# Kernel optimization log

Measured on AMD Instinct MI355X. Metric: run time of the kernel, lower is better.

## Reference

```python
import jax, jax.numpy as jnp
import numpy as np

B, S, D = 4, 1024, 2048
H, KVH = 32, 8
HD = D // H            # 64
KVD = HD * KVH         # 512
RANK, ALPHA = 16, 32
LORA_SCALE = ALPHA / RANK


def setup_inputs() -> dict:
    key = jax.random.key(0)
    ks = jax.random.split(key, 14)
    x = jax.random.normal(ks[0], (B, S, D), dtype=jnp.float32)
    # RoPE tables (llama-style complex freqs as cos/sin)
    inv = 1.0 / (10000.0 ** (np.arange(0, HD, 2, dtype=np.float32) / HD))
    t = np.arange(S, dtype=np.float32)
    ang = np.outer(t, inv)  # [S, HD//2]
    freqs_cos = jnp.asarray(np.cos(ang))
    freqs_sin = jnp.asarray(np.sin(ang))
    s = 0.02
    Wq = jax.random.normal(ks[1], (D, D), dtype=jnp.float32) * s
    Wk = jax.random.normal(ks[2], (D, KVD), dtype=jnp.float32) * s
    Wv = jax.random.normal(ks[3], (D, KVD), dtype=jnp.float32) * s
    Wo = jax.random.normal(ks[4], (D, D), dtype=jnp.float32) * s
    qA = jax.random.normal(ks[5], (D, RANK), dtype=jnp.float32) * s
    qB = jax.random.normal(ks[6], (RANK, D), dtype=jnp.float32) * s
    kA = jax.random.normal(ks[7], (D, RANK), dtype=jnp.float32) * s
    kB = jax.random.normal(ks[8], (RANK, KVD), dtype=jnp.float32) * s
    vA = jax.random.normal(ks[9], (D, RANK), dtype=jnp.float32) * s
    vB = jax.random.normal(ks[10], (RANK, KVD), dtype=jnp.float32) * s
    return {"x": x, "freqs_cos": freqs_cos, "freqs_sin": freqs_sin,
            "Wq": Wq, "Wk": Wk, "Wv": Wv, "Wo": Wo,
            "qA": qA, "qB": qB, "kA": kA, "kB": kB, "vA": vA, "vB": vB}


def _rope(t, cos, sin):
    # t: [b, s, h, hd]; cos/sin: [s, hd//2]
    b, s, h, hd = t.shape
    t2 = t.reshape(b, s, h, hd // 2, 2)
    x0, x1 = t2[..., 0], t2[..., 1]
    c = cos[None, :, None, :]
    sn = sin[None, :, None, :]
    r0 = x0 * c - x1 * sn
    r1 = x0 * sn + x1 * c
    return jnp.stack([r0, r1], axis=-1).reshape(b, s, h, hd)


def reference(x, freqs_cos, freqs_sin, Wq, Wk, Wv, Wo, qA, qB, kA, kB, vA, vB):
    b, s, _ = x.shape
    # QKV projections + LoRA deltas
    q = x @ Wq + (x @ qA) @ qB * LORA_SCALE   # [b,s,D]
    k = x @ Wk + (x @ kA) @ kB * LORA_SCALE   # [b,s,KVD]
    v = x @ Wv + (x @ vA) @ vB * LORA_SCALE   # [b,s,KVD]
    q = q.reshape(b, s, H, HD)
    k = k.reshape(b, s, KVH, HD)
    v = v.reshape(b, s, KVH, HD)
    q = _rope(q, freqs_cos, freqs_sin)
    k = _rope(k, freqs_cos, freqs_sin)
    # GQA attention without materializing repeated K/V:
    rep = H // KVH
    qg = q.reshape(b, s, KVH, rep, HD)
    scale = 1.0 / jnp.sqrt(jnp.asarray(HD, dtype=x.dtype))
    scores = jnp.einsum('bsgrd,btgd->bgrst', qg, k) * scale  # [b,kvh,rep,s,s]
    causal = jnp.tril(jnp.ones((s, s), dtype=bool))
    scores = jnp.where(causal[None, None, None], scores, jnp.finfo(scores.dtype).min)
    attn = jax.nn.softmax(scores, axis=-1)
    ctx = jnp.einsum('bgrst,btgd->bsgrd', attn, v).reshape(b, s, D)
    return ctx @ Wo
```

## Files before the change

### kernel.cpp

```cpp
#include <hip/hip_runtime.h>

typedef unsigned short u16;
typedef unsigned int u32;
typedef __attribute__((ext_vector_type(8))) short short8;
typedef __attribute__((ext_vector_type(4))) float f32x4;
typedef __attribute__((ext_vector_type(4))) u16 u16x4;

#define LOG2E 1.4426950408889634f
#define SCL2 (0.125f * LOG2E)

static __device__ __forceinline__ float bf2f(u16 u) {
    return __uint_as_float(((unsigned)u) << 16);
}
static __device__ __forceinline__ u16 f2bf(float f) {
    unsigned u = __float_as_uint(f);
    unsigned r = (u + 0x7FFF + ((u >> 16) & 1)) >> 16;
    return (u16)r;
}
static __device__ __forceinline__ u32 cvtpk(float lo, float hi) {
    u32 r;
    asm("v_cvt_pk_bf16_f32 %0, %1, %2" : "=v"(r) : "v"(lo), "v"(hi));
    return r;
}
static __device__ __forceinline__ f32x4 mfma16(short8 a, short8 b, f32x4 c) {
    return __builtin_amdgcn_mfma_f32_16x16x32_bf16(a, b, c, 0, 0, 0);
}
static __device__ __forceinline__ void gload_lds16(const void* g, void* l) {
    __builtin_amdgcn_global_load_lds(
        (const __attribute__((address_space(1))) void*)g,
        (__attribute__((address_space(3))) void*)l, 16, 0, 0);
}

#define GBAR() do { asm volatile("" ::: "memory"); __builtin_amdgcn_s_barrier(); asm volatile("" ::: "memory"); } while (0)
#define LGW()  do { asm volatile("s_waitcnt lgkmcnt(0)" ::: "memory"); __builtin_amdgcn_sched_barrier(0); } while (0)

__global__ void cast_pack_kernel(const float* __restrict__ x, u16* __restrict__ xb,
                                 const float* __restrict__ cosb, const float* __restrict__ sinb,
                                 u32* __restrict__ tbl) {
    if (blockIdx.x >= 2048) {
        const int i = (blockIdx.x - 2048) * 1024 + threadIdx.x * 4;
#pragma unroll
        for (int j = 0; j < 4; ++j)
            tbl[i + j] = (u32)f2bf(cosb[i + j]) | ((u32)f2bf(sinb[i + j]) << 16);
        return;
    }
    constexpr int n = 4096 * 2048;
    constexpr int stride = 2048 * 256 * 4;
    int i = (blockIdx.x * 256 + threadIdx.x) * 4;
#pragma unroll
    for (; i < n; i += stride) {
        f32x4 v = *(const f32x4*)&x[i];
        u16x4 o;
        o.x = f2bf(v.x); o.y = f2bf(v.y); o.z = f2bf(v.z); o.w = f2bf(v.w);
        *(u16x4*)&xb[i] = o;
    }
}

__global__ void prep_weights_kernel(
    const float* __restrict__ Wq, const float* __restrict__ Wk,
    const float* __restrict__ Wv, const float* __restrict__ Wo,
    const float* __restrict__ qA, const float* __restrict__ qB,
    const float* __restrict__ kA, const float* __restrict__ kB,
    const float* __restrict__ vA, const float* __restrict__ vB,
    u16* __restrict__ WqkvT, u16* __restrict__ WoT) {
    __shared__ float tile[32][33];
    __shared__ float As[32][17];
    __shared__ float Bs[16][33];
    const int id = blockIdx.x;
    const int tx = threadIdx.x, ty = threadIdx.y;
    const float *W, *A = nullptr, *Bm = nullptr;
    u16* dst;
    int C, bx, by;
    bool fold = true;
    if (id < 4096)      { W = Wq; A = qA; Bm = qB; dst = WqkvT; C = 2048; bx = id & 63; by = id >> 6; }
    else if (id < 5120) { int t = id - 4096; W = Wk; A = kA; Bm = kB; dst = WqkvT + (size_t)2048 * 2048; C = 512; bx = t & 15; by = t >> 4; }
    else if (id < 6144) { int t = id - 5120; W = Wv; A = vA; Bm = vB; dst = WqkvT + (size_t)2560 * 2048; C = 512; bx = t & 15; by = t >> 4; }
    else                { int t = id - 6144; W = Wo; dst = WoT; C = 2048; bx = t & 63; by = t >> 6; fold = false; }
    const int c0 = bx * 32, r0 = by * 32;
    tile[ty][tx] = W[(size_t)(r0 + ty) * C + c0 + tx];
    if (fold) {
        if (tx < 16) As[ty][tx] = A[(r0 + ty) * 16 + tx];
        if (ty < 16) Bs[ty][tx] = Bm[(size_t)ty * C + c0 + tx];
    }
    __syncthreads();
    float v = tile[tx][ty];
    if (fold) {
        float acc = 0.0f;
#pragma unroll
        for (int rr = 0; rr < 16; ++rr) acc += As[tx][rr] * Bs[rr][ty];
        v += 2.0f * acc;
    }
    dst[(size_t)(c0 + ty) * 2048 + r0 + tx] = f2bf(v);
}

__global__ __launch_bounds__(512) void gemm256_qkv_kernel(
    const u16* __restrict__ A, const u16* __restrict__ Bt, u16* __restrict__ Cq,
    u16* __restrict__ Ck, u16* __restrict__ Vt, const u32* __restrict__ ropetbl) {
    constexpr int K = 2048, NT = 32;
    __shared__ u16 Asl[2][256 * 64];
    __shared__ u16 Bsl[2][192 * 64];
    const int tid = threadIdx.x;
    const int wid = tid >> 6, lane = tid & 63;
    const int flat = blockIdx.x;
    const int m = ((flat & 7) << 1) + ((flat >> 3) & 1);
    const int n = flat >> 4;
    const int mbase = m * 256, nbase = n * 192;
    const int wrow = (wid >> 2) * 128, wcol = (wid & 3) * 48;
    const int fr = lane & 15, hi = lane >> 4;
    const int rs2 = fr & 7;
    f32x4 acc[8][3] = {};
    short8 Af[4][2], Bf[3][2];
    const u16* Ag = A + (size_t)mbase * K;
    const u16* Bg = Bt + (size_t)nbase * K;

    auto HT = [&](int t, int j) {
        if (t >= NT) return;
        const int buf = t & 1;
        const bool isA = (j < 4);
        u16* l = isA ? &Asl[buf][0] : &Bsl[buf][0];
        const u16* g = isA ? Ag : Bg;
        const int rbase = (isA ? j : (j - 4)) * 64;
        const int row = rbase + (tid >> 3);
        const int sl = (tid & 7) ^ ((tid >> 3) & 7);
        gload_lds16(&g[(size_t)row * K + t * 64 + sl * 8],
                    &l[rbase * 64 + wid * 512]);
    };
    auto DSA = [&](int mo, int buf) {
#pragma unroll
        for (int mi = 0; mi < 4; ++mi)
#pragma unroll
            for (int ks = 0; ks < 2; ++ks)
                Af[mi][ks] = *(const short8*)&Asl[buf][(wrow + (mo + mi) * 16 + fr) * 64 +
                                                       (((ks * 4 + hi) ^ rs2) * 8)];
    };
    auto DSB = [&](int nlo, int nhi, int buf) {
#pragma unroll
        for (int ni = 0; ni < 3; ++ni) {
            if (ni < nlo || ni >= nhi) continue;
#pragma unroll
            for (int ks = 0; ks < 2; ++ks)
                Bf[ni][ks] = *(const short8*)&Bsl[buf][(wcol + ni * 16 + fr) * 64 +
                                                       (((ks * 4 + hi) ^ rs2) * 8)];
        }
    };
    auto MFq = [&](int mo, int nlo, int nhi) {
        __builtin_amdgcn_s_setprio(1);
#pragma unroll
        for (int mi = 0; mi < 4; ++mi)
#pragma unroll
            for (int ni = 0; ni < 3; ++ni) {
                if (ni < nlo || ni >= nhi) continue;
#pragma unroll
                for (int ks = 0; ks < 2; ++ks)
                    acc[mo + mi][ni] = mfma16(Af[mi][ks], Bf[ni][ks], acc[mo + mi][ni]);
            }
        __builtin_amdgcn_s_setprio(0);
    };

    HT(0, 0); HT(0, 1); HT(0, 2); HT(0, 3); HT(0, 4); HT(0, 5); HT(0, 6);
    HT(1, 0); HT(1, 1); HT(1, 2); HT(1, 3);
    asm volatile("s_waitcnt vmcnt(4)" ::: "memory");
    GBAR();

#pragma unroll 1
    for (int i = 0; i < NT / 2; ++i) {
        const int t = 2 * i;
        DSA(0, 0); DSB(0, 2, 0); HT(t + 1, 4); HT(t + 1, 5);
        GBAR(); LGW(); MFq(0, 0, 2); GBAR();
        DSB(2, 3, 0); HT(t + 1, 6);
        GBAR(); LGW(); MFq(0, 2, 3); GBAR();
        DSA(4, 0);
        GBAR(); LGW(); MFq(4, 0, 2); GBAR();
        HT(t + 2, 0); HT(t + 2, 1); HT(t + 2, 2); HT(t + 2, 3);
        GBAR(); LGW(); MFq(4, 2, 3);
        if (t + 2 < NT) { asm volatile("s_waitcnt vmcnt(4)" ::: "memory"); }
        else            { asm volatile("s_waitcnt vmcnt(0)" ::: "memory"); }
        GBAR();
        DSA(0, 1); DSB(0, 2, 1); HT(t + 2, 4); HT(t + 2, 5);
        GBAR(); LGW(); MFq(0, 0, 2); GBAR();
        DSB(2, 3, 1); HT(t + 2, 6);
        GBAR(); LGW(); MFq(0, 2, 3); GBAR();
        DSA(4, 1);
        GBAR(); LGW(); MFq(4, 0, 2); GBAR();
        HT(t + 3, 0); HT(t + 3, 1); HT(t + 3, 2); HT(t + 3, 3);
        GBAR(); LGW(); MFq(4, 2, 3);
        if (t + 3 < NT)          { asm volatile("s_waitcnt vmcnt(4)" ::: "memory"); }
        else if (i < NT / 2 - 1) { asm volatile("s_waitcnt vmcnt(0)" ::: "memory"); }
        GBAR();
    }

    const int rb = mbase + wrow + (hi << 2);
#pragma unroll
    for (int ni = 0; ni < 3; ++ni) {
        const int colc = nbase + wcol + ni * 16;
        if (colc >= 2560) {
            const int feat = colc - 2560 + fr;
#pragma unroll
            for (int mi = 0; mi < 8; ++mi) {
                u16x4 w;
#pragma unroll
                for (int j = 0; j < 4; ++j) w[j] = f2bf(acc[mi][ni][j]);
                *(u16x4*)&Vt[(size_t)feat * 4096 + rb + mi * 16] = w;
            }
        } else {
            u16* C; int cs, ccol; float scale;
            if (colc < 2048) { C = Cq; cs = 2048; ccol = colc + fr;        scale = SCL2; }
            else             { C = Ck; cs = 512;  ccol = colc - 2048 + fr; scale = 1.0f; }
            const bool odd = (lane & 1);
            const int i0 = ((colc & 63) >> 1) + (fr >> 1);
#pragma unroll
            for (int mi = 0; mi < 8; ++mi)
#pragma unroll
                for (int j = 0; j < 4; ++j) {
                    const int row = rb + mi * 16 + j;
                    u32 cspk = ropetbl[(row & 1023) * 32 + i0];
                    float cv = bf2f((u16)cspk), sv = bf2f((u16)(cspk >> 16));
                    float v = acc[mi][ni][j];
                    float p = __shfl_xor(v, 1);
                    float r = odd ? (p * sv + v * cv) : (v * cv - p * sv);
                    C[(size_t)row * cs + ccol] = f2bf(r * scale);
                }
        }
    }
}

template <int CN>
__global__ __launch_bounds__(256) void gemm_kernel(
    const u16* __restrict__ A, const u16* __restrict__ Bt, float* __restrict__ C0, int Nn) {
    constexpr int K = 2048;
    constexpr int NT = K / 64;
    __shared__ u16 As[2][128 * 64];
    __shared__ u16 Bs[2][128 * 64];
    const int tid = threadIdx.x;
    const int wid = tid >> 6, lane = tid & 63;
    const int flat = blockIdx.y * gridDim.x + blockIdx.x;
    const int xcd = flat & 7, local = flat >> 3;
    const int mbase = (((xcd & 3) << 3) + (local & 7)) * 128;
    const int nbase = ((xcd >> 2) * CN + (local >> 3)) * 128;
    const int wrow = (wid >> 1) * 64, wcol = (wid & 1) * 64;
    const int fr = lane & 15, hi = lane >> 4;
    const int l8 = lane >> 3;
    const int swc = ((lane & 7) ^ l8) * 8;
    const int rs = fr & 7;
    f32x4 acc[4][4] = {};
    const u16* Ag = A + (size_t)mbase * K;
    const u16* Bg = Bt + (size_t)nbase * K;

    auto STAGE = [&](int kt, int buf) {
#pragma unroll
        for (int i = 0; i < 4; ++i) {
            const int r8 = (i * 4 + wid) * 8;
            gload_lds16(&Ag[(size_t)(r8 + l8) * K + kt * 64 + swc], &As[buf][r8 * 64]);
            gload_lds16(&Bg[(size_t)(r8 + l8) * K + kt * 64 + swc], &Bs[buf][r8 * 64]);
        }
    };

    STAGE(0, 0);
    for (int kt = 0; kt < NT; ++kt) {
        const int cur = kt & 1;
        if (kt < NT - 1) {
            STAGE(kt + 1, cur ^ 1);
            asm volatile("s_waitcnt vmcnt(8)" ::: "memory");
        } else {
            asm volatile("s_waitcnt vmcnt(0)" ::: "memory");
        }
        __builtin_amdgcn_s_barrier();
#pragma unroll
        for (int ks = 0; ks < 2; ++ks) {
            short8 af[4], bfr[4];
#pragma unroll
            for (int i = 0; i < 4; ++i) {
                const int arow = wrow + i * 16 + fr;
                const int brow = wcol + i * 16 + fr;
                af[i]  = *(const short8*)&As[cur][arow * 64 + (((ks * 4 + hi) ^ rs) * 8)];
                bfr[i] = *(const short8*)&Bs[cur][brow * 64 + (((ks * 4 + hi) ^ rs) * 8)];
            }
#pragma unroll
            for (int mi = 0; mi < 4; ++mi)
#pragma unroll
                for (int ni = 0; ni < 4; ++ni)
                    acc[mi][ni] = mfma16(af[mi], bfr[ni], acc[mi][ni]);
        }
        __builtin_amdgcn_s_barrier();
    }
    const int rb = mbase + wrow + (hi << 2);
    const int cb = nbase + wcol + fr;
#pragma unroll
    for (int mi = 0; mi < 4; ++mi)
#pragma unroll
        for (int j = 0; j < 4; ++j) {
            const size_t ro = (size_t)(rb + mi * 16 + j) * Nn;
#pragma unroll
            for (int ni = 0; ni < 4; ++ni) C0[ro + cb + ni * 16] = acc[mi][ni][j];
        }
}

template <bool DIAG>
static __device__ __forceinline__ void attn_tile_step(
    const u16* __restrict__ Ksb, const u16* __restrict__ Vsb,
    const short8* qf, f32x4* o, float& m, float& l,
    int sq, int kvb, int wid, int fr, int hi) {
    f32x4 s[4];
    const int sw = fr & 7;
#pragma unroll
    for (int mi = 0; mi < 4; ++mi) {
        if (!DIAG || mi <= wid) {
            const int row = (mi * 16 + fr) * 64;
            short8 kf0 = *(const short8*)&Ksb[row + ((hi ^ sw) * 8)];
            short8 kf1 = *(const short8*)&Ksb[row + (((4 + hi) ^ sw) * 8)];
            f32x4 z = {};
            z = mfma16(kf0, qf[0], z);
            z = mfma16(kf1, qf[1], z);
#pragma unroll
            for (int j = 0; j < 4; ++j) {
                float val = z[j];
                if (DIAG && mi == wid && (kvb + mi * 16 + hi * 4 + j > sq)) val = -3.0e38f;
                s[mi][j] = val;
            }
        } else {
            s[mi][0] = -3.0e38f; s[mi][1] = -3.0e38f;
            s[mi][2] = -3.0e38f; s[mi][3] = -3.0e38f;
        }
    }
    float pmax = fmaxf(fmaxf(fmaxf(s[0][0], s[0][1]), fmaxf(s[0][2], s[0][3])),
                       fmaxf(fmaxf(s[1][0], s[1][1]), fmaxf(s[1][2], s[1][3])));
    pmax = fmaxf(pmax, fmaxf(fmaxf(fmaxf(s[2][0], s[2][1]), fmaxf(s[2][2], s[2][3])),
                             fmaxf(fmaxf(s[3][0], s[3][1]), fmaxf(s[3][2], s[3][3]))));
    pmax = fmaxf(pmax, __shfl_xor(pmax, 16));
    pmax = fmaxf(pmax, __shfl_xor(pmax, 32));
    if (__any(pmax > m + 8.0f)) {
        const float mnew = fmaxf(m, pmax);
        const float fsc = exp2f(m - mnew);
        l *= fsc;
        m = mnew;
#pragma unroll
        for (int dn = 0; dn < 4; ++dn)
#pragma unroll
            for (int j = 0; j < 4; ++j) o[dn][j] *= fsc;
    }
    float rs = 0.0f;
    u32 pk[4][2];
#pragma unroll
    for (int mi = 0; mi < 4; ++mi) {
        float p0 = exp2f(s[mi][0] - m);
        float p1 = exp2f(s[mi][1] - m);
        float p2 = exp2f(s[mi][2] - m);
        float p3 = exp2f(s[mi][3] - m);
        rs += (p0 + p1) + (p2 + p3);
        pk[mi][0] = cvtpk(p0, p1);
        pk[mi][1] = cvtpk(p2, p3);
    }
    rs += __shfl_xor(rs, 16);
    rs += __shfl_xor(rs, 32);
    l += rs;
    const int ksmax = DIAG ? (wid >> 1) : 1;
#pragma unroll
    for (int ks = 0; ks < 2; ++ks) {
        if (ks > ksmax) continue;
        u32 w0 = pk[2 * ks][0], w2 = pk[2 * ks + 1][0];
        u32 w1 = pk[2 * ks][1], w3 = pk[2 * ks + 1][1];
        asm volatile("v_permlane32_swap_b32 %0, %1" : "+v"(w0), "+v"(w2));
        asm volatile("v_permlane16_swap_b32 %0, %1" : "+v"(w0), "+v"(w2));
        asm volatile("v_permlane32_swap_b32 %0, %1" : "+v"(w1), "+v"(w3));
        asm volatile("v_permlane16_swap_b32 %0, %1" : "+v"(w1), "+v"(w3));
        union { u32 w[4]; short8 s8; } pu;
        pu.w[0] = w0; pu.w[1] = w1; pu.w[2] = w2; pu.w[3] = w3;
        short8 pf = pu.s8;
#pragma unroll
        for (int dn = 0; dn < 4; ++dn) {
            const int row = (dn * 16 + fr) * 64;
            short8 vf = *(const short8*)&Vsb[row + (((ks * 4 + hi) ^ sw) * 8)];
            o[dn] = mfma16(vf, pf, o[dn]);
        }
    }
}

__global__ __launch_bounds__(256) void attn_kernel(
    const u16* __restrict__ q, const u16* __restrict__ k, const u16* __restrict__ vt,
    u16* __restrict__ ctx) {
    __shared__ u16 Ks[2][64 * 64];
    __shared__ u16 Vs[2][64 * 64];
    const int flat = blockIdx.x + 8 * (blockIdx.y + 16 * blockIdx.z);
    const int c = flat & 7, t = flat >> 3;
    const int jp = t & 7;
    const int grp = c + 8 * (t >> 3);
    const int hp = grp & 15, b = grp >> 4;
    const int qtA = jp, qtB = 15 - jp;
    const int h0 = hp * 2;
    const int g = hp >> 1;
    const int tid = threadIdx.x, wid = tid >> 6, lane = tid & 63;
    const int fr = lane & 15, hi = lane >> 4, fk = hi * 8;
    const int sqA = qtA * 64 + wid * 16 + fr;
    const int sqB = qtB * 64 + wid * 16 + fr;
    short8 qA0[2], qB0[2], qA1[2], qB1[2];
    {
        const u16* pa = &q[((size_t)(b * 1024 + sqA)) * 2048 + h0 * 64];
        qA0[0] = *(const short8*)&pa[fk];      qA0[1] = *(const short8*)&pa[32 + fk];
        qA1[0] = *(const short8*)&pa[64 + fk]; qA1[1] = *(const short8*)&pa[96 + fk];
        const u16* pb = &q[((size_t)(b * 1024 + sqB)) * 2048 + h0 * 64];
        qB0[0] = *(const short8*)&pb[fk];      qB0[1] = *(const short8*)&pb[32 + fk];
        qB1[0] = *(const short8*)&pb[64 + fk]; qB1[1] = *(const short8*)&pb[96 + fk];
    }
    f32x4 oA0[4] = {}, oA1[4] = {}, oB0[4] = {}, oB1[4] = {};
    float mA0 = -3.0e38f, lA0 = 0.0f, mA1 = -3.0e38f, lA1 = 0.0f;
    float mB0 = -3.0e38f, lB0 = 0.0f, mB1 = -3.0e38f, lB1 = 0.0f;
    const u16* kbase = k + ((size_t)b * 1024) * 512 + g * 64;
    const u16* vbase = vt + ((size_t)(g * 64)) * 4096 + b * 1024;
    const int l8 = lane >> 3;
    const int sw8 = ((lane & 7) ^ l8) * 8;

    auto stage = [&](int kt, int buf) {
        const u16* kg = kbase + (size_t)(kt * 64) * 512;
        const u16* vg = vbase + kt * 64;
#pragma unroll
        for (int i = 0; i < 2; ++i) {
            const int r8 = (i * 4 + wid) * 8;
            gload_lds16(&kg[(size_t)(r8 + l8) * 512 + sw8], &Ks[buf][r8 * 64]);
            gload_lds16(&vg[(size_t)(r8 + l8) * 4096 + sw8], &Vs[buf][r8 * 64]);
        }
    };

    stage(0, 0);
    for (int kt = 0; kt <= qtB; ++kt) {
        const int cur = kt & 1;
        __syncthreads();
        if (kt < qtB) stage(kt + 1, cur ^ 1);
        const int kvb = kt * 64;
        if (kt < qtA) {
            attn_tile_step<false>(Ks[cur], Vs[cur], qA0, oA0, mA0, lA0, sqA, kvb, wid, fr, hi);
            attn_tile_step<false>(Ks[cur], Vs[cur], qA1, oA1, mA1, lA1, sqA, kvb, wid, fr, hi);
        } else if (kt == qtA) {
            attn_tile_step<true>(Ks[cur], Vs[cur], qA0, oA0, mA0, lA0, sqA, kvb, wid, fr, hi);
            attn_tile_step<true>(Ks[cur], Vs[cur], qA1, oA1, mA1, lA1, sqA, kvb, wid, fr, hi);
        }
        if (kt < qtB) {
            attn_tile_step<false>(Ks[cur], Vs[cur], qB0, oB0, mB0, lB0, sqB, kvb, wid, fr, hi);
            attn_tile_step<false>(Ks[cur], Vs[cur], qB1, oB1, mB1, lB1, sqB, kvb, wid, fr, hi);
        } else {
            attn_tile_step<true>(Ks[cur], Vs[cur], qB0, oB0, mB0, lB0, sqB, kvb, wid, fr, hi);
            attn_tile_step<true>(Ks[cur], Vs[cur], qB1, oB1, mB1, lB1, sqB, kvb, wid, fr, hi);
        }
    }
    auto emit = [&](const f32x4* o, float l, int sq, int h) {
        const float linv = 1.0f / l;
        const size_t obase = ((size_t)(b * 1024 + sq)) * 2048 + h * 64;
#pragma unroll
        for (int dn = 0; dn < 4; ++dn) {
            u16x4 w;
#pragma unroll
            for (int j = 0; j < 4; ++j) w[j] = f2bf(o[dn][j] * linv);
            *(u16x4*)&ctx[obase + dn * 16 + hi * 4] = w;
        }
    };
    emit(oA0, lA0, sqA, h0);
    emit(oA1, lA1, sqA, h0 + 1);
    emit(oB0, lB0, sqB, h0);
    emit(oB1, lB1, sqB, h0 + 1);
}

extern "C" void kernel_launch(void* const* d_in, const int* in_sizes, int n_in,
                              void* d_out, int out_size, void* d_ws, size_t ws_size,
                              hipStream_t stream) {
    const float* x    = (const float*)d_in[0];
    const float* fcos = (const float*)d_in[1];
    const float* fsin = (const float*)d_in[2];
    const float* Wq   = (const float*)d_in[3];
    const float* Wk   = (const float*)d_in[4];
    const float* Wv   = (const float*)d_in[5];
    const float* Wo   = (const float*)d_in[6];
    const float* qA   = (const float*)d_in[7];
    const float* qB   = (const float*)d_in[8];
    const float* kA   = (const float*)d_in[9];
    const float* kB   = (const float*)d_in[10];
    const float* vA   = (const float*)d_in[11];
    const float* vB   = (const float*)d_in[12];
    float* out = (float*)d_out;

    char* ws = (char*)d_ws;
    size_t off = 0;
    auto alloc = [&](size_t bytes) { char* p = ws + off; off += (bytes + 255) & ~(size_t)255; return p; };
    u16* xb     = (u16*)alloc((size_t)4096 * 2048 * 2);
    u16* WqkvT  = (u16*)alloc((size_t)3072 * 2048 * 2);
    u16* WoT    = (u16*)alloc((size_t)2048 * 2048 * 2);
    u16* qbuf   = (u16*)alloc((size_t)4096 * 2048 * 2);
    u16* kbuf   = (u16*)alloc((size_t)4096 * 512 * 2);
    u16* VT2    = (u16*)alloc((size_t)512 * 4096 * 2);
    u16* ctx    = (u16*)alloc((size_t)4096 * 2048 * 2);
    u32* rtbl   = (u32*)alloc((size_t)1024 * 32 * 4);

    cast_pack_kernel<<<2080, 256, 0, stream>>>(x, xb, fcos, fsin, rtbl);
    prep_weights_kernel<<<10240, dim3(32, 32), 0, stream>>>(
        Wq, Wk, Wv, Wo, qA, qB, kA, kB, vA, vB, WqkvT, WoT);

    gemm256_qkv_kernel<<<dim3(256), 512, 0, stream>>>(xb, WqkvT, qbuf, kbuf, VT2, rtbl);

    attn_kernel<<<dim3(8, 16, 4), 256, 0, stream>>>(qbuf, kbuf, VT2, ctx);

    gemm_kernel<8><<<dim3(32, 16), 256, 0, stream>>>(ctx, WoT, out, 2048);
}
```

Measured before the change: 194.0 us.

## Replace Wo projection GEMM with 256x128 tiled, 8-wave pipelined kernel

Replaces the 128x128 four-wave output-projection GEMM with a 256x128 tile kernel that uses eight waves and 256 blocks. Global-to-LDS loads are split into pieces and interleaved with MFMA quarters under fine-grained barriers and s_setprio, modeled on the existing QKV kernel. The larger tile lowers global traffic per FLOP and the interleaving aims to hide load latency, at the cost of more LDS, more barriers, and a hard-coded grid mapping.

New measurement: 199.0 us. 1.03x slower.

```diff
diff --git a/kernel.cpp b/kernel.cpp
--- a/kernel.cpp
+++ b/kernel.cpp
@@ -224,74 +224,102 @@
     }
 }
 
-template <int CN>
-__global__ __launch_bounds__(256) void gemm_kernel(
-    const u16* __restrict__ A, const u16* __restrict__ Bt, float* __restrict__ C0, int Nn) {
-    constexpr int K = 2048;
-    constexpr int NT = K / 64;
-    __shared__ u16 As[2][128 * 64];
-    __shared__ u16 Bs[2][128 * 64];
+__global__ __launch_bounds__(512) void gemm256_wo_kernel(
+    const u16* __restrict__ A, const u16* __restrict__ Bt, float* __restrict__ Cf) {
+    constexpr int K = 2048, NT = 32;
+    __shared__ u16 Asl[2][256 * 64];
+    __shared__ u16 Bsl[2][128 * 64];
     const int tid = threadIdx.x;
     const int wid = tid >> 6, lane = tid & 63;
-    const int flat = blockIdx.y * gridDim.x + blockIdx.x;
-    const int xcd = flat & 7, local = flat >> 3;
-    const int mbase = (((xcd & 3) << 3) + (local & 7)) * 128;
-    const int nbase = ((xcd >> 2) * CN + (local >> 3)) * 128;
-    const int wrow = (wid >> 1) * 64, wcol = (wid & 1) * 64;
+    const int flat = blockIdx.x;
+    const int m = ((flat & 7) << 1) + ((flat >> 3) & 1);
+    const int n = flat >> 4;
+    const int mbase = m * 256, nbase = n * 128;
+    const int wrow = (wid >> 2) * 128, wcol = (wid & 3) * 32;
     const int fr = lane & 15, hi = lane >> 4;
-    const int l8 = lane >> 3;
-    const int swc = ((lane & 7) ^ l8) * 8;
-    const int rs = fr & 7;
-    f32x4 acc[4][4] = {};
+    const int rs2 = fr & 7;
+    f32x4 acc[8][2] = {};
+    short8 Af[4][2], Bf[2][2];
     const u16* Ag = A + (size_t)mbase * K;
     const u16* Bg = Bt + (size_t)nbase * K;
 
-    auto STAGE = [&](int kt, int buf) {
-#pragma unroll
-        for (int i = 0; i < 4; ++i) {
-            const int r8 = (i * 4 + wid) * 8;
-            gload_lds16(&Ag[(size_t)(r8 + l8) * K + kt * 64 + swc], &As[buf][r8 * 64]);
-            gload_lds16(&Bg[(size_t)(r8 + l8) * K + kt * 64 + swc], &Bs[buf][r8 * 64]);
-        }
-    };
-
-    STAGE(0, 0);
-    for (int kt = 0; kt < NT; ++kt) {
-        const int cur = kt & 1;
-        if (kt < NT - 1) {
-            STAGE(kt + 1, cur ^ 1);
-            asm volatile("s_waitcnt vmcnt(8)" ::: "memory");
-        } else {
-            asm volatile("s_waitcnt vmcnt(0)" ::: "memory");
-        }
-        __builtin_amdgcn_s_barrier();
-#pragma unroll
-        for (int ks = 0; ks < 2; ++ks) {
-            short8 af[4], bfr[4];
-#pragma unroll
-            for (int i = 0; i < 4; ++i) {
-                const int arow = wrow + i * 16 + fr;
-                const int brow = wcol + i * 16 + fr;
-                af[i]  = *(const short8*)&As[cur][arow * 64 + (((ks * 4 + hi) ^ rs) * 8)];
-                bfr[i] = *(const short8*)&Bs[cur][brow * 64 + (((ks * 4 + hi) ^ rs) * 8)];
-            }
-#pragma unroll
-            for (int mi = 0; mi < 4; ++mi)
-#pragma unroll
-                for (int ni = 0; ni < 4; ++ni)
-                    acc[mi][ni] = mfma16(af[mi], bfr[ni], acc[mi][ni]);
-        }
-        __builtin_amdgcn_s_barrier();
-    }
+    auto HT = [&](int t, int j) {
+        if (t >= NT) return;
+        const int buf = t & 1;
+        const bool isA = (j < 4);
+        u16* l = isA ? &Asl[buf][0] : &Bsl[buf][0];
+        const u16* g = isA ? Ag : Bg;
+        const int rbase = (isA ? j : (j - 4)) * 64;
+        const int row = rbase + (tid >> 3);
+        const int sl = (tid & 7) ^ ((tid >> 3) & 7);
+        gload_lds16(&g[(size_t)row * K + t * 64 + sl * 8],
+                    &l[rbase * 64 + wid * 512]);
+    };
+    auto DSA = [&](int mo, int buf) {
+#pragma unroll
+        for (int mi = 0; mi < 4; ++mi)
+#pragma unroll
+            for (int ks = 0; ks < 2; ++ks)
+                Af[mi][ks] = *(const short8*)&Asl[buf][(wrow + (mo + mi) * 16 + fr) * 64 +
+                                                       (((ks * 4 + hi) ^ rs2) * 8)];
+    };
+    auto DSB = [&](int buf) {
+#pragma unroll
+        for (int ni = 0; ni < 2; ++ni)
+#pragma unroll
+            for (int ks = 0; ks < 2; ++ks)
+                Bf[ni][ks] = *(const short8*)&Bsl[buf][(wcol + ni * 16 + fr) * 64 +
+                                                       (((ks * 4 + hi) ^ rs2) * 8)];
+    };
+    auto MFq = [&](int mo, int ni) {
+        __builtin_amdgcn_s_setprio(1);
+#pragma unroll
+        for (int mi = 0; mi < 4; ++mi)
+#pragma unroll
+            for (int ks = 0; ks < 2; ++ks)
+                acc[mo + mi][ni] = mfma16(Af[mi][ks], Bf[ni][ks], acc[mo + mi][ni]);
+        __builtin_amdgcn_s_setprio(0);
+    };
+
+    HT(0, 0); HT(0, 1); HT(0, 2); HT(0, 3); HT(0, 4); HT(0, 5);
+    HT(1, 0); HT(1, 1); HT(1, 2); HT(1, 3);
+    asm volatile("s_waitcnt vmcnt(4)" ::: "memory");
+    GBAR();
+
+#pragma unroll 1
+    for (int i = 0; i < NT / 2; ++i) {
+        const int t = 2 * i;
+        DSA(0, 0); DSB(0); HT(t + 1, 4); HT(t + 1, 5);
+        GBAR(); LGW(); MFq(0, 0); GBAR();
+        GBAR(); LGW(); MFq(0, 1); GBAR();
+        DSA(4, 0);
+        GBAR(); LGW(); MFq(4, 0); GBAR();
+        HT(t + 2, 0); HT(t + 2, 1); HT(t + 2, 2); HT(t + 2, 3);
+        GBAR(); LGW(); MFq(4, 1);
+        if (t + 2 < NT) { asm volatile("s_waitcnt vmcnt(4)" ::: "memory"); }
+        else            { asm volatile("s_waitcnt vmcnt(0)" ::: "memory"); }
+        GBAR();
+        DSA(0, 1); DSB(1); HT(t + 2, 4); HT(t + 2, 5);
+        GBAR(); LGW(); MFq(0, 0); GBAR();
+        GBAR(); LGW(); MFq(0, 1); GBAR();
+        DSA(4, 1);
+        GBAR(); LGW(); MFq(4, 0); GBAR();
+        HT(t + 3, 0); HT(t + 3, 1); HT(t + 3, 2); HT(t + 3, 3);
+        GBAR(); LGW(); MFq(4, 1);
+        if (t + 3 < NT)          { asm volatile("s_waitcnt vmcnt(4)" ::: "memory"); }
+        else if (i < NT / 2 - 1) { asm volatile("s_waitcnt vmcnt(0)" ::: "memory"); }
+        GBAR();
+    }
+
     const int rb = mbase + wrow + (hi << 2);
     const int cb = nbase + wcol + fr;
 #pragma unroll
-    for (int mi = 0; mi < 4; ++mi)
+    for (int mi = 0; mi < 8; ++mi)
 #pragma unroll
         for (int j = 0; j < 4; ++j) {
-            const size_t ro = (size_t)(rb + mi * 16 + j) * Nn;
-#pragma unroll
-            for (int ni = 0; ni < 4; ++ni) C0[ro + cb + ni * 16] = acc[mi][ni][j];
+            const size_t ro = (size_t)(rb + mi * 16 + j) * 2048;
+#pragma unroll
+            for (int ni = 0; ni < 2; ++ni) Cf[ro + cb + ni * 16] = acc[mi][ni][j];
         }
 }
 
@@ -496,5 +524,5 @@
 
     attn_kernel<<<dim3(8, 16, 4), 256, 0, stream>>>(qbuf, kbuf, VT2, ctx);
 
-    gemm_kernel<8><<<dim3(32, 16), 256, 0, stream>>>(ctx, WoT, out, 2048);
-}
+    gemm256_wo_kernel<<<dim3(256), 512, 0, stream>>>(ctx, WoT, out);
+}
```
